# Optimization experiments

Hardware: AMD Instinct MI355X
Metric: run time of the kernel (lower is better)

## Reference

```python
import jax, jax.numpy as jnp
import numpy as np

N_HEAD = 16
EPS = 1e-06


def setup_inputs() -> dict:
    key = jax.random.key(0)
    ks = jax.random.split(key, 9)
    B, S, Q, D, Dp = 16, 4096, 49, 1024, 1024
    INIT = 0.02  # GPT-2 style init scale keeps exp(scores) finite
    x = jax.random.normal(ks[0], (B, S, D), dtype=jnp.float32)
    y = jax.random.normal(ks[1], (B, Q, Dp), dtype=jnp.float32)
    # multiplicative binary mask applied to exp(scores), shaped [1,1,49,S//64,64]
    attention_mask = (jax.random.uniform(ks[2], (1, 1, Q, S // 64, 64)) > 0.5).astype(jnp.float32)
    W_attn = jax.random.normal(ks[3], (D, 2 * D), dtype=jnp.float32) * INIT
    b_attn = jnp.zeros((2 * D,), dtype=jnp.float32)
    W_mlp = jax.random.normal(ks[4], (Dp, D), dtype=jnp.float32) * INIT
    b_mlp = jnp.zeros((D,), dtype=jnp.float32)
    W_proj = jax.random.normal(ks[5], (D, Dp), dtype=jnp.float32) * INIT
    b_proj = jnp.zeros((Dp,), dtype=jnp.float32)
    return {"x": x, "y": y, "attention_mask": attention_mask,
            "W_attn": W_attn, "b_attn": b_attn, "W_mlp": W_mlp, "b_mlp": b_mlp,
            "W_proj": W_proj, "b_proj": b_proj}


def reference(x, y, attention_mask, W_attn, b_attn, W_mlp, b_mlp, W_proj, b_proj):
    B, S, D = x.shape
    Q = y.shape[1]
    H = N_HEAD
    hd = D // H
    # c_attn (Conv1D): x @ W + b -> split into key, value
    kv = x @ W_attn + b_attn                       # [B,S,2D]
    key, value = kv[..., :D], kv[..., D:]
    k = key.reshape(B, S, H, hd).transpose(0, 2, 3, 1)    # [B,H,hd,S] (k=True perm)
    v = value.reshape(B, S, H, hd).transpose(0, 2, 1, 3)  # [B,H,S,hd]
    q = (y @ W_mlp + b_mlp).reshape(B, Q, H, hd).transpose(0, 2, 1, 3)  # [B,H,Q,hd]
    # fp32 scores, scaled by sqrt(head_dim)
    w = jnp.einsum('bhqd,bhds->bhqs', q.astype(jnp.float32), k.astype(jnp.float32))
    w = w / jnp.sqrt(jnp.float32(hd))
    # custom exp + multiplicative blocked mask + epsilon-stabilized normalize
    e = (jnp.exp(w).reshape(B, H, 49, -1, 64) * attention_mask).reshape(B, H, Q, S)
    w = e / (e.sum(-1, keepdims=True) + EPS)
    # PV matmul, cast to bf16 as in the original, then merge heads
    a = jnp.einsum('bhqs,bhsd->bhqd', w, v.astype(jnp.float32)).astype(jnp.bfloat16)
    a = a.transpose(0, 2, 1, 3).reshape(B, Q, D).astype(jnp.float32)
    out = a @ W_proj + b_proj                      # c_proj
    return out
```

## Files before the change

kernel.cpp:

```cpp
#include <hip/hip_runtime.h>
#include <cstdint>

typedef __bf16 bf16x8 __attribute__((ext_vector_type(8)));
typedef float f32x4 __attribute__((ext_vector_type(4)));
typedef unsigned short u16;

#define GBAR() asm volatile("s_barrier" ::: "memory")
#define SBAR0() __builtin_amdgcn_sched_barrier(0)
#define LGKM0() do { asm volatile("s_waitcnt lgkmcnt(0)" ::: "memory"); SBAR0(); } while (0)
#define VM6()  asm volatile("s_waitcnt vmcnt(6)" ::: "memory")
#define VM8()  asm volatile("s_waitcnt vmcnt(8)" ::: "memory")
#define MFMA16(a, b, c) __builtin_amdgcn_mfma_f32_16x16x32_bf16((a), (b), (c), 0, 0, 0)

__device__ __forceinline__ u16 f2bf(float f) {
  unsigned u = __builtin_bit_cast(unsigned, f);
  u += 0x7fffu + ((u >> 16) & 1u);
  return (u16)(u >> 16);
}
__device__ __forceinline__ float bfu(ushort4 v, int r) {
  unsigned short s = (r == 0) ? v.x : (r == 1) ? v.y : (r == 2) ? v.z : v.w;
  return __builtin_bit_cast(float, (unsigned)s << 16);
}

__global__ void cast_f32_bf16(const float* __restrict__ in, u16* __restrict__ out,
                              int n4) {
  int i = blockIdx.x * blockDim.x + threadIdx.x;
  int stride = gridDim.x * blockDim.x;
  for (; i < n4; i += stride) {
    float4 v = ((const float4*)in)[i];
    ushort4 o;
    o.x = f2bf(v.x); o.y = f2bf(v.y); o.z = f2bf(v.z); o.w = f2bf(v.w);
    ((ushort4*)out)[i] = o;
  }
}

__global__ void transpose_all(const float* __restrict__ Wa, const float* __restrict__ Wm,
                              const float* __restrict__ Wp,
                              u16* __restrict__ oa, u16* __restrict__ om,
                              u16* __restrict__ op) {
  __shared__ float t[64][65];
  int z = blockIdx.z;
  const float* in = (z == 0) ? Wa : (z == 1) ? Wm : Wp;
  u16* out = (z == 0) ? oa : (z == 1) ? om : op;
  int C = (z == 0) ? 2048 : 1024;
  const int R = 1024;
  if (blockIdx.x * 64 >= C) return;
  int tc = blockIdx.x * 64, tr = blockIdx.y * 64;
  int c = threadIdx.x & 63, r0 = threadIdx.x >> 6;
  #pragma unroll
  for (int p = 0; p < 16; ++p) {
    int r = p * 4 + r0;
    t[r][c] = in[(long)(tr + r) * C + (tc + c)];
  }
  __syncthreads();
  #pragma unroll
  for (int p = 0; p < 16; ++p) {
    int r = p * 4 + r0;
    out[(long)(tc + r) * R + (tr + c)] = f2bf(t[c][r]);
  }
}

__global__ void mask_prep(const float* __restrict__ in, u16* __restrict__ out) {
  __shared__ float t[64][65];
  int s0 = blockIdx.x * 64;
  int c = threadIdx.x & 63, r0 = threadIdx.x >> 6;
  #pragma unroll
  for (int p = 0; p < 16; ++p) {
    int q = p * 4 + r0;
    t[q][c] = (q < 49) ? in[(long)q * 4096 + s0 + c] : 0.f;
  }
  __syncthreads();
  #pragma unroll
  for (int p = 0; p < 16; ++p) {
    int r = p * 4 + r0;
    out[(long)(s0 + r) * 64 + c] = f2bf(t[c][r]);
  }
}

template<int MODE>
__global__ __launch_bounds__(512, 2) void gemm256(
    const u16* __restrict__ A, const u16* __restrict__ BT,
    const float* __restrict__ bias, void* __restrict__ outp)
{
  __shared__ __align__(16) char lds[131072];

  int tid = threadIdx.x;
  int l = tid & 63, w = tid >> 6;
  int wr = w >> 2, wc = w & 3;
  int lr = l & 15, lh = l >> 4;

  int bid = blockIdx.x;
  int mt, nt;
  long out_off = 0;
  const u16* Ap = A;
  const u16* BTp = BT;
  if constexpr (MODE == 0) {
    int wg = (bid & 7) * 128 + (bid >> 3);
    mt = wg >> 2; nt = wg & 3;
  } else {
    int wg = (bid & 7) * 8 + (bid >> 3);
    mt = wg & 3; nt = wg >> 2;
    int b = blockIdx.y;
    BTp = BT + (long)b * 4194304;
    out_off = (long)b * 4194304;
  }
  long Arow0 = (long)mt * 256;
  long Brow0 = (long)nt * 256;

  int rho = (w << 3) + (l >> 3);
  int csw = ((l & 7) ^ (l >> 3)) << 3;
  const u16* agA = Ap + (Arow0 + rho) * 1024 + csw;
  int browoff = (w >> 2) * 64 + (w & 3) * 8 + (l >> 3);
  const u16* agB = BTp + (Brow0 + browoff) * 1024 + csw;
  char* ldsAthr = lds + rho * 128 + (l & 7) * 16;
  char* ldsBthr = lds + 32768 + browoff * 128 + (l & 7) * 16;

  auto SA = [&](int dt, int st, int mh) {
    char* d = ldsAthr + (dt & 1) * 65536 + mh * 8192;
    const u16* s = agA + (long)st * 64 + mh * 65536;
    __builtin_amdgcn_global_load_lds(
        (const __attribute__((address_space(1))) void*)s,
        (__attribute__((address_space(3))) void*)d, 16, 0, 0);
    __builtin_amdgcn_global_load_lds(
        (const __attribute__((address_space(1))) void*)(s + 131072),
        (__attribute__((address_space(3))) void*)(d + 16384), 16, 0, 0);
  };
  auto SB = [&](int dt, int st, int h) {
    char* d = ldsBthr + (dt & 1) * 65536 + h * 4096;
    const u16* s = agB + (long)st * 64 + h * 32768;
    __builtin_amdgcn_global_load_lds(
        (const __attribute__((address_space(1))) void*)s,
        (__attribute__((address_space(3))) void*)d, 16, 0, 0);
    __builtin_amdgcn_global_load_lds(
        (const __attribute__((address_space(1))) void*)(s + 131072),
        (__attribute__((address_space(3))) void*)(d + 16384), 16, 0, 0);
  };

  int arow_b = (wr * 128 + lr) * 128;
  int brow_b = (wc * 64 + lr) * 128 + 32768;
  int xr0 = (lh ^ (lr & 7)) << 4;
  int xr1 = ((4 + lh) ^ (lr & 7)) << 4;

  f32x4 acc[8][4];
  #pragma unroll
  for (int m = 0; m < 8; ++m)
    #pragma unroll
    for (int n = 0; n < 4; ++n) acc[m][n] = f32x4{0.f, 0.f, 0.f, 0.f};

  bf16x8 af[4][2], bn0[2][2], bn1[2][2];

  auto RD_AF0 = [&](int buf) {
    #pragma unroll
    for (int m = 0; m < 4; ++m) {
      af[m][0] = *(const bf16x8*)(lds + buf + arow_b + m * 2048 + xr0);
      af[m][1] = *(const bf16x8*)(lds + buf + arow_b + m * 2048 + xr1);
    }
  };
  auto RD_AF1 = [&](int buf) {
    #pragma unroll
    for (int m = 0; m < 4; ++m) {
      af[m][0] = *(const bf16x8*)(lds + buf + arow_b + 8192 + m * 2048 + xr0);
      af[m][1] = *(const bf16x8*)(lds + buf + arow_b + 8192 + m * 2048 + xr1);
    }
  };
  auto RD_BN0 = [&](int buf) {
    #pragma unroll
    for (int n = 0; n < 2; ++n) {
      bn0[n][0] = *(const bf16x8*)(lds + buf + brow_b + n * 2048 + xr0);
      bn0[n][1] = *(const bf16x8*)(lds + buf + brow_b + n * 2048 + xr1);
    }
  };
  auto RD_BN1 = [&](int buf) {
    #pragma unroll
    for (int n = 0; n < 2; ++n) {
      bn1[n][0] = *(const bf16x8*)(lds + buf + brow_b + 4096 + n * 2048 + xr0);
      bn1[n][1] = *(const bf16x8*)(lds + buf + brow_b + 4096 + n * 2048 + xr1);
    }
  };
  auto Q = [&](int mo, int no, bf16x8 (&bn)[2][2]) {
    __builtin_amdgcn_s_setprio(1);
    #pragma unroll
    for (int m = 0; m < 4; ++m)
      #pragma unroll
      for (int n = 0; n < 2; ++n) {
        acc[mo + m][no + n] = MFMA16(af[m][0], bn[n][0], acc[mo + m][no + n]);
        acc[mo + m][no + n] = MFMA16(af[m][1], bn[n][1], acc[mo + m][no + n]);
      }
    __builtin_amdgcn_s_setprio(0);
  };

  SA(0, 0, 0); SA(0, 0, 1); SB(0, 0, 0); SB(0, 0, 1);
  SA(1, 1, 0); SA(1, 1, 1); SB(1, 1, 0);
  VM6(); GBAR();

  for (int i = 0; i < 8; ++i) {
    int t = 2 * i;
    RD_AF0(0); RD_BN0(0); SBAR0();
    SB(t + 1, t + 1, 1);
    GBAR(); LGKM0();
    Q(0, 0, bn0);
    GBAR();
    RD_BN1(0); SBAR0();
    { int tt = t + 2; SA(tt, tt < 16 ? tt : 15, 0); }
    GBAR(); LGKM0();
    Q(0, 2, bn1);
    GBAR();
    RD_AF1(0); SBAR0();
    { int tt = t + 2; SB(tt, tt < 16 ? tt : 15, 0); }
    GBAR(); LGKM0();
    Q(4, 0, bn0);
    GBAR();
    { int tt = t + 2; SA(tt, tt < 16 ? tt : 15, 1); }
    GBAR(); VM6();
    Q(4, 2, bn1);
    GBAR();
    RD_AF0(65536); RD_BN0(65536); SBAR0();
    { int tt = t + 2; SB(tt, tt < 16 ? tt : 15, 1); }
    GBAR(); LGKM0();
    Q(0, 0, bn0);
    GBAR();
    RD_BN1(65536); SBAR0();
    { int tt = t + 3; SA(tt, tt < 16 ? tt : 15, 0); }
    GBAR(); LGKM0();
    Q(0, 2, bn1);
    GBAR();
    RD_AF1(65536); SBAR0();
    { int tt = t + 3; SB(tt, tt < 16 ? tt : 15, 0); }
    GBAR(); LGKM0();
    Q(4, 0, bn0);
    GBAR();
    { int tt = t + 3; SA(tt, tt < 16 ? tt : 15, 1); }
    GBAR(); VM6();
    Q(4, 2, bn1);
    GBAR();
  }

  asm volatile("s_waitcnt vmcnt(0)" ::: "memory");

  #pragma unroll
  for (int m = 0; m < 8; ++m) {
    #pragma unroll
    for (int n = 0; n < 4; ++n) {
      #pragma unroll
      for (int r = 0; r < 4; ++r) {
        long row = Arow0 + wr * 128 + m * 16 + lh * 4 + r;
        long col = Brow0 + wc * 64 + n * 16 + lr;
        float v = acc[m][n][r];
        if constexpr (MODE == 0) {
          v += bias[col];
          long addr = (row >> 12) * 4194304 + (col >> 6) * 262144
                    + (row & 4095) * 64 + (col & 63);
          ((u16*)outp)[addr] = f2bf(v);
        } else {
          v += bias[1024 + row];
          ((u16*)outp)[out_off + row * 4096 + col] = f2bf(v);
        }
      }
    }
  }
}

template<int MODE>
__global__ __launch_bounds__(256, 4) void gemm64(
    const void* __restrict__ Ap, const u16* __restrict__ BT,
    const float* __restrict__ bias, void* __restrict__ outp)
{
  __shared__ u16 As[64][64];
  __shared__ u16 Bs[64][64];

  int bid = blockIdx.x;
  int mt = bid >> 4, nt = bid & 15;
  int tid = threadIdx.x;
  int l = tid & 63, w = tid >> 6;
  int wr = w >> 1, wc = w & 1;
  int lr = l & 15, lh = l >> 4;

  f32x4 acc[2][2];
  #pragma unroll
  for (int m = 0; m < 2; ++m)
    #pragma unroll
    for (int n = 0; n < 2; ++n) acc[m][n] = f32x4{0.f, 0.f, 0.f, 0.f};

  long arow0 = (long)mt * 64;
  long brow0 = (long)nt * 64;
  int srow = tid >> 3, sc = tid & 7;

  for (int kt = 0; kt < 16; ++kt) {
    int ko = kt * 64;
    #pragma unroll
    for (int p = 0; p < 2; ++p) {
      int row = srow + p * 32;
      int cs = (sc ^ (row & 7)) << 3;
      __builtin_amdgcn_global_load_lds(
          (const __attribute__((address_space(1))) void*)(BT + (brow0 + row) * 1024 + ko + cs),
          (__attribute__((address_space(3))) void*)(&Bs[row][sc * 8]), 16, 0, 0);
      if constexpr (MODE == 3)
        __builtin_amdgcn_global_load_lds(
            (const __attribute__((address_space(1))) void*)((const u16*)Ap + (arow0 + row) * 1024 + ko + cs),
            (__attribute__((address_space(3))) void*)(&As[row][sc * 8]), 16, 0, 0);
    }
    if constexpr (MODE == 2) {
      #pragma unroll
      for (int p = 0; p < 2; ++p) {
        int row = srow + p * 32;
        int cs = (sc ^ (row & 7)) << 3;
        ushort4 o0 = {0, 0, 0, 0}, o1 = {0, 0, 0, 0};
        if (arow0 + row < 784) {
          const float* src = (const float*)Ap + (arow0 + row) * 1024 + ko + cs;
          float4 f0 = *(const float4*)src;
          float4 f1 = *(const float4*)(src + 4);
          o0.x = f2bf(f0.x); o0.y = f2bf(f0.y); o0.z = f2bf(f0.z); o0.w = f2bf(f0.w);
          o1.x = f2bf(f1.x); o1.y = f2bf(f1.y); o1.z = f2bf(f1.z); o1.w = f2bf(f1.w);
        }
        *(ushort4*)(&As[row][sc * 8]) = o0;
        *(ushort4*)(&As[row][sc * 8 + 4]) = o1;
      }
    }
    __syncthreads();
    #pragma unroll
    for (int kk = 0; kk < 2; ++kk) {
      bf16x8 afr[2], bfr[2];
      #pragma unroll
      for (int m = 0; m < 2; ++m) {
        int row = wr * 32 + m * 16 + lr;
        afr[m] = *(const bf16x8*)((const char*)&As[row][0] + (((kk * 4 + lh) ^ (row & 7)) << 4));
      }
      #pragma unroll
      for (int n = 0; n < 2; ++n) {
        int row = wc * 32 + n * 16 + lr;
        bfr[n] = *(const bf16x8*)((const char*)&Bs[row][0] + (((kk * 4 + lh) ^ (row & 7)) << 4));
      }
      #pragma unroll
      for (int m = 0; m < 2; ++m)
        #pragma unroll
        for (int n = 0; n < 2; ++n)
          acc[m][n] = MFMA16(afr[m], bfr[n], acc[m][n]);
    }
    __syncthreads();
  }

  #pragma unroll
  for (int m = 0; m < 2; ++m) {
    #pragma unroll
    for (int n = 0; n < 2; ++n) {
      #pragma unroll
      for (int r = 0; r < 4; ++r) {
        int row = (int)arow0 + wr * 32 + m * 16 + lh * 4 + r;
        int col = (int)brow0 + wc * 32 + n * 16 + lr;
        if (row < 784) {
          float v = acc[m][n][r] + bias[col];
          if constexpr (MODE == 2) {
            int b = row / 49, qi = row - b * 49;
            long addr = ((long)(b * 16 + (col >> 6)) * 64 + qi) * 64 + (col & 63);
            ((u16*)outp)[addr] = f2bf(v);
          } else {
            ((float*)outp)[(long)row * 1024 + col] = v;
          }
        }
      }
    }
  }
}

__global__ __launch_bounds__(256, 4) void attn_part(
    const u16* __restrict__ Kt, const u16* __restrict__ Vt, const u16* __restrict__ Q,
    const u16* __restrict__ maskT,
    float* __restrict__ partA, float* __restrict__ prs)
{
  __shared__ __align__(16) char lds[40960];

  int bh = blockIdx.x, chunk = blockIdx.y;
  int tid = threadIdx.x;
  int l = tid & 63, w = tid >> 6;
  int lr = l & 15, lh = l >> 4;

  const u16* Kb = Kt + (long)bh * 262144;
  const u16* Vb = Vt + (long)bh * 262144;
  const u16* Qb = Q + (long)bh * 4096;

  int t0 = chunk * 16;
  const int nt = 16;
  int tmax = t0 + nt - 1;

  int strow = tid >> 3;
  int sc = tid & 7;

  auto STAGE = [&](int buf, int tt) {
    long s0 = (long)tt * 64;
    #pragma unroll
    for (int h = 0; h < 2; ++h) {
      int row = h * 32 + strow;
      int cs = (sc ^ (row & 7)) << 3;
      const u16* ksrc = Kb + (s0 + row) * 64 + cs;
      char* kdst = lds + buf * 8192 + row * 128 + sc * 16;
      __builtin_amdgcn_global_load_lds(
          (const __attribute__((address_space(1))) void*)ksrc,
          (__attribute__((address_space(3))) void*)kdst, 16, 0, 0);
      const u16* vsrc = Vb + (long)row * 4096 + s0 + cs;
      char* vdst = lds + 16384 + buf * 8192 + row * 128 + sc * 16;
      __builtin_amdgcn_global_load_lds(
          (const __attribute__((address_space(1))) void*)vsrc,
          (__attribute__((address_space(3))) void*)vdst, 16, 0, 0);
    }
  };

  bf16x8 qf[2];
  #pragma unroll
  for (int kf2 = 0; kf2 < 2; ++kf2)
    qf[kf2] = *(const bf16x8*)(Qb + (w * 16 + lr) * 64 + kf2 * 32 + lh * 8);

  bf16x8 ones;
  #pragma unroll
  for (int j = 0; j < 8; ++j) ones[j] = (__bf16)1.0f;

  f32x4 acc_a[4];
  #pragma unroll
  for (int n = 0; n < 4; ++n) acc_a[n] = f32x4{0.f, 0.f, 0.f, 0.f};
  f32x4 acc_rs = f32x4{0.f, 0.f, 0.f, 0.f};

  char* Pw = lds + 32768 + w * 2048;
  const u16* mbase = maskT + w * 16 + lh * 4;

  STAGE(0, t0);
  STAGE(1, t0 + 1);
  ushort4 mvu[4];
  #pragma unroll
  for (int sf = 0; sf < 4; ++sf)
    mvu[sf] = *(const ushort4*)(mbase + ((long)t0 * 64 + sf * 16 + lr) * 64);
  VM8();
  GBAR();

  for (int it = 0; it < nt; ++it) {
    int buf = it & 1;
    const char* Kl = lds + buf * 8192;
    const char* Vl = lds + 16384 + buf * 8192;

    int tn = it + 1 < nt ? t0 + it + 1 : tmax;
    ushort4 mvn[4];
    #pragma unroll
    for (int sf = 0; sf < 4; ++sf)
      mvn[sf] = *(const ushort4*)(mbase + ((long)tn * 64 + sf * 16 + lr) * 64);

    bf16x8 kf[4][2];
    #pragma unroll
    for (int sf = 0; sf < 4; ++sf) {
      int srw = sf * 16 + lr;
      int xb = srw & 7;
      kf[sf][0] = *(const bf16x8*)(Kl + srw * 128 + ((lh ^ xb) << 4));
      kf[sf][1] = *(const bf16x8*)(Kl + srw * 128 + (((4 + lh) ^ xb) << 4));
    }
    f32x4 lg[4];
    #pragma unroll
    for (int sf = 0; sf < 4; ++sf) {
      f32x4 t = f32x4{0.f, 0.f, 0.f, 0.f};
      t = MFMA16(qf[0], kf[sf][0], t);
      t = MFMA16(qf[1], kf[sf][1], t);
      lg[sf] = t;
    }

    bf16x8 vf[2][4];
    #pragma unroll
    for (int k2 = 0; k2 < 2; ++k2)
      #pragma unroll
      for (int n = 0; n < 4; ++n) {
        int vrow = n * 16 + lr;
        vf[k2][n] = *(const bf16x8*)(Vl + vrow * 128 + (((k2 * 4 + lh) ^ (lr & 7)) << 4));
      }

    #pragma unroll
    for (int sf = 0; sf < 4; ++sf) {
      #pragma unroll
      for (int r = 0; r < 4; ++r) {
        int qq = lh * 4 + r;
        float e = __expf(lg[sf][r] * 0.125f) * bfu(mvu[sf], r);
        int byte = (qq * 128 + (sf * 16 + lr) * 2) ^ ((qq & 7) << 4);
        *(u16*)(Pw + byte) = f2bf(e);
      }
    }

    #pragma unroll
    for (int k2 = 0; k2 < 2; ++k2) {
      int byte = (lr * 128 + k2 * 64 + lh * 16) ^ ((lr & 7) << 4);
      bf16x8 pf;
      __builtin_memcpy(&pf, Pw + byte, 16);
      #pragma unroll
      for (int n = 0; n < 4; ++n)
        acc_a[n] = MFMA16(pf, vf[k2][n], acc_a[n]);
      acc_rs = MFMA16(pf, ones, acc_rs);
    }

    LGKM0();
    GBAR();
    { int tt = it + 2 < nt ? t0 + it + 2 : tmax; STAGE(buf, tt); }
    VM8();
    GBAR();

    #pragma unroll
    for (int sf = 0; sf < 4; ++sf) mvu[sf] = mvn[sf];
  }

  long base = ((long)bh * 4 + chunk) * 64;
  #pragma unroll
  for (int r = 0; r < 4; ++r) {
    int q = w * 16 + lh * 4 + r;
    if (lr == 0) prs[base + q] = acc_rs[r];
    #pragma unroll
    for (int n = 0; n < 4; ++n)
      partA[(base + q) * 64 + n * 16 + lr] = acc_a[n][r];
  }
}

__global__ __launch_bounds__(256) void attn_reduce(
    const float* __restrict__ partA, const float* __restrict__ prs,
    u16* __restrict__ Abf)
{
  int bh = blockIdx.x;
  int t = threadIdx.x;
  int q = t >> 2, d0 = (t & 3) * 16;
  if (q >= 49) return;
  int b = bh >> 4, h = bh & 15;

  float rs = 1e-6f;
  #pragma unroll
  for (int c = 0; c < 4; ++c) rs += prs[((long)bh * 4 + c) * 64 + q];

  #pragma unroll
  for (int j = 0; j < 4; ++j) {
    float4 s = float4{0.f, 0.f, 0.f, 0.f};
    #pragma unroll
    for (int c = 0; c < 4; ++c) {
      float4 v = *(const float4*)(partA + (((long)bh * 4 + c) * 64 + q) * 64 + d0 + j * 4);
      s.x += v.x; s.y += v.y; s.z += v.z; s.w += v.w;
    }
    ushort4 o;
    o.x = f2bf(s.x / rs); o.y = f2bf(s.y / rs);
    o.z = f2bf(s.z / rs); o.w = f2bf(s.w / rs);
    *(ushort4*)(Abf + ((long)(b * 49 + q) * 1024 + h * 64 + d0 + j * 4)) = o;
  }
}

extern "C" void kernel_launch(void* const* d_in, const int* in_sizes, int n_in,
                              void* d_out, int out_size, void* d_ws, size_t ws_size,
                              hipStream_t stream) {
  const float* x      = (const float*)d_in[0];
  const float* y      = (const float*)d_in[1];
  const float* mask   = (const float*)d_in[2];
  const float* W_attn = (const float*)d_in[3];
  const float* b_attn = (const float*)d_in[4];
  const float* W_mlp  = (const float*)d_in[5];
  const float* b_mlp  = (const float*)d_in[6];
  const float* W_proj = (const float*)d_in[7];
  const float* b_proj = (const float*)d_in[8];

  if (ws_size < 417333248ULL) return;

  char* ws = (char*)d_ws;
  u16* x_bf    = (u16*)(ws);
  u16* Kt      = (u16*)(ws + 134217728L);
  u16* Vt      = (u16*)(ws + 268435456L);
  u16* WT_attn = (u16*)(ws + 402653184L);
  u16* WT_mlp  = (u16*)(ws + 406847488L);
  u16* WT_proj = (u16*)(ws + 408944640L);
  u16* q_ws    = (u16*)(ws + 412876800L);
  u16* a_bf    = (u16*)(ws + 414973952L);
  u16* maskT   = (u16*)(ws + 416808960L);
  float* partA = (float*)(ws);
  float* prs   = (float*)(ws + 16777216L);

  cast_f32_bf16<<<2048, 256, 0, stream>>>(x, x_bf, 16777216);
  transpose_all<<<dim3(32, 16, 3), 256, 0, stream>>>(W_attn, W_mlp, W_proj,
                                                     WT_attn, WT_mlp, WT_proj);
  mask_prep<<<64, 256, 0, stream>>>(mask, maskT);

  gemm256<0><<<1024, 512, 0, stream>>>(x_bf, WT_attn, b_attn, Kt);
  gemm256<1><<<dim3(64, 16), 512, 0, stream>>>(WT_attn + 1048576, x_bf, b_attn, Vt);
  gemm64<2><<<224, 256, 0, stream>>>(y, WT_mlp, b_mlp, q_ws);

  attn_part<<<dim3(256, 4), 256, 0, stream>>>(Kt, Vt, q_ws, maskT, partA, prs);
  attn_reduce<<<256, 256, 0, stream>>>(partA, prs, a_bf);

  gemm64<3><<<224, 256, 0, stream>>>(a_bf, WT_proj, b_proj, d_out);
}
```

Baseline: 465.4 us.

## Stage only activation tile in LDS with triple buffering, read weights from global

The 256x256 bf16 GEMM now copies only the activation operand into LDS, using three 32KB buffers filled with global_load_lds two k-steps ahead. The weight operand fragments are loaded straight from global memory into registers each k-step. The fine-grained half-tile schedule with many barriers becomes one loop step per 64-wide k-slice with a single barrier. This cuts LDS footprint, LDS traffic and barrier count, but exposes global-load latency on the weight fragments. It also relies on implicit vmcnt waits to make sure the staged LDS buffers have landed before they are read.

```diff
diff --git a/kernel.cpp b/kernel.cpp
--- a/kernel.cpp
+++ b/kernel.cpp
@@ -8,7 +8,6 @@
 #define GBAR() asm volatile("s_barrier" ::: "memory")
 #define SBAR0() __builtin_amdgcn_sched_barrier(0)
 #define LGKM0() do { asm volatile("s_waitcnt lgkmcnt(0)" ::: "memory"); SBAR0(); } while (0)
-#define VM6()  asm volatile("s_waitcnt vmcnt(6)" ::: "memory")
 #define VM8()  asm volatile("s_waitcnt vmcnt(8)" ::: "memory")
 #define MFMA16(a, b, c) __builtin_amdgcn_mfma_f32_16x16x32_bf16((a), (b), (c), 0, 0, 0)
 
@@ -82,7 +81,7 @@
     const u16* __restrict__ A, const u16* __restrict__ BT,
     const float* __restrict__ bias, void* __restrict__ outp)
 {
-  __shared__ __align__(16) char lds[131072];
+  __shared__ __align__(16) char lds[98304];
 
   int tid = threadIdx.x;
   int l = tid & 63, w = tid >> 6;
@@ -107,37 +106,29 @@
   long Arow0 = (long)mt * 256;
   long Brow0 = (long)nt * 256;
 
+  const u16* xbase = (MODE == 0) ? Ap : BTp;
+  long xrow0 = (MODE == 0) ? Arow0 : Brow0;
   int rho = (w << 3) + (l >> 3);
   int csw = ((l & 7) ^ (l >> 3)) << 3;
-  const u16* agA = Ap + (Arow0 + rho) * 1024 + csw;
-  int browoff = (w >> 2) * 64 + (w & 3) * 8 + (l >> 3);
-  const u16* agB = BTp + (Brow0 + browoff) * 1024 + csw;
-  char* ldsAthr = lds + rho * 128 + (l & 7) * 16;
-  char* ldsBthr = lds + 32768 + browoff * 128 + (l & 7) * 16;
-
-  auto SA = [&](int dt, int st, int mh) {
-    char* d = ldsAthr + (dt & 1) * 65536 + mh * 8192;
-    const u16* s = agA + (long)st * 64 + mh * 65536;
-    __builtin_amdgcn_global_load_lds(
-        (const __attribute__((address_space(1))) void*)s,
-        (__attribute__((address_space(3))) void*)d, 16, 0, 0);
-    __builtin_amdgcn_global_load_lds(
-        (const __attribute__((address_space(1))) void*)(s + 131072),
-        (__attribute__((address_space(3))) void*)(d + 16384), 16, 0, 0);
+  const u16* xg = xbase + (xrow0 + rho) * 1024 + csw;
+  char* ldsthr = lds + rho * 128 + (l & 7) * 16;
+
+  auto STAGE_X = [&](int bi, int st) {
+    char* d = ldsthr + bi * 32768;
+    const u16* s = xg + (long)st * 64;
+    #pragma unroll
+    for (int q = 0; q < 4; ++q)
+      __builtin_amdgcn_global_load_lds(
+          (const __attribute__((address_space(1))) void*)(s + (long)q * 65536),
+          (__attribute__((address_space(3))) void*)(d + q * 8192), 16, 0, 0);
   };
-  auto SB = [&](int dt, int st, int h) {
-    char* d = ldsBthr + (dt & 1) * 65536 + h * 4096;
-    const u16* s = agB + (long)st * 64 + h * 32768;
-    __builtin_amdgcn_global_load_lds(
-        (const __attribute__((address_space(1))) void*)s,
-        (__attribute__((address_space(3))) void*)d, 16, 0, 0);
-    __builtin_amdgcn_global_load_lds(
-        (const __attribute__((address_space(1))) void*)(s + 131072),
-        (__attribute__((address_space(3))) void*)(d + 16384), 16, 0, 0);
-  };
+
+  const u16* wgp = (MODE == 0)
+      ? BTp + (Brow0 + wc * 64 + lr) * 1024 + lh * 8
+      : Ap  + (Arow0 + wr * 128 + lr) * 1024 + lh * 8;
 
   int arow_b = (wr * 128 + lr) * 128;
-  int brow_b = (wc * 64 + lr) * 128 + 32768;
+  int brow_b = (wc * 64 + lr) * 128;
   int xr0 = (lh ^ (lr & 7)) << 4;
   int xr1 = ((4 + lh) ^ (lr & 7)) << 4;
 
@@ -149,34 +140,6 @@
 
   bf16x8 af[4][2], bn0[2][2], bn1[2][2];
 
-  auto RD_AF0 = [&](int buf) {
-    #pragma unroll
-    for (int m = 0; m < 4; ++m) {
-      af[m][0] = *(const bf16x8*)(lds + buf + arow_b + m * 2048 + xr0);
-      af[m][1] = *(const bf16x8*)(lds + buf + arow_b + m * 2048 + xr1);
-    }
-  };
-  auto RD_AF1 = [&](int buf) {
-    #pragma unroll
-    for (int m = 0; m < 4; ++m) {
-      af[m][0] = *(const bf16x8*)(lds + buf + arow_b + 8192 + m * 2048 + xr0);
-      af[m][1] = *(const bf16x8*)(lds + buf + arow_b + 8192 + m * 2048 + xr1);
-    }
-  };
-  auto RD_BN0 = [&](int buf) {
-    #pragma unroll
-    for (int n = 0; n < 2; ++n) {
-      bn0[n][0] = *(const bf16x8*)(lds + buf + brow_b + n * 2048 + xr0);
-      bn0[n][1] = *(const bf16x8*)(lds + buf + brow_b + n * 2048 + xr1);
-    }
-  };
-  auto RD_BN1 = [&](int buf) {
-    #pragma unroll
-    for (int n = 0; n < 2; ++n) {
-      bn1[n][0] = *(const bf16x8*)(lds + buf + brow_b + 4096 + n * 2048 + xr0);
-      bn1[n][1] = *(const bf16x8*)(lds + buf + brow_b + 4096 + n * 2048 + xr1);
-    }
-  };
   auto Q = [&](int mo, int no, bf16x8 (&bn)[2][2]) {
     __builtin_amdgcn_s_setprio(1);
     #pragma unroll
@@ -189,53 +152,70 @@
     __builtin_amdgcn_s_setprio(0);
   };
 
-  SA(0, 0, 0); SA(0, 0, 1); SB(0, 0, 0); SB(0, 0, 1);
-  SA(1, 1, 0); SA(1, 1, 1); SB(1, 1, 0);
-  VM6(); GBAR();
-
-  for (int i = 0; i < 8; ++i) {
-    int t = 2 * i;
-    RD_AF0(0); RD_BN0(0); SBAR0();
-    SB(t + 1, t + 1, 1);
-    GBAR(); LGKM0();
-    Q(0, 0, bn0);
+  STAGE_X(0, 0);
+  STAGE_X(1, 1);
+  asm volatile("s_waitcnt vmcnt(4)" ::: "memory");
+  GBAR();
+
+  int cur = 0;
+  for (int t = 0; t < 16; ++t) {
+    int buf = cur * 32768;
+    if constexpr (MODE == 0) {
+      #pragma unroll
+      for (int n = 0; n < 2; ++n)
+        #pragma unroll
+        for (int h = 0; h < 2; ++h) {
+          bn0[n][h] = *(const bf16x8*)(wgp + n * 16384 + t * 64 + h * 32);
+          bn1[n][h] = *(const bf16x8*)(wgp + (n + 2) * 16384 + t * 64 + h * 32);
+        }
+      SBAR0();
+      #pragma unroll
+      for (int m = 0; m < 4; ++m) {
+        af[m][0] = *(const bf16x8*)(lds + buf + arow_b + m * 2048 + xr0);
+        af[m][1] = *(const bf16x8*)(lds + buf + arow_b + m * 2048 + xr1);
+      }
+      LGKM0();
+      Q(0, 0, bn0); Q(0, 2, bn1);
+      #pragma unroll
+      for (int m = 0; m < 4; ++m) {
+        af[m][0] = *(const bf16x8*)(lds + buf + arow_b + 8192 + m * 2048 + xr0);
+        af[m][1] = *(const bf16x8*)(lds + buf + arow_b + 8192 + m * 2048 + xr1);
+      }
+      LGKM0();
+      Q(4, 0, bn0); Q(4, 2, bn1);
+    } else {
+      #pragma unroll
+      for (int m = 0; m < 4; ++m)
+        #pragma unroll
+        for (int h = 0; h < 2; ++h)
+          af[m][h] = *(const bf16x8*)(wgp + m * 16384 + t * 64 + h * 32);
+      SBAR0();
+      #pragma unroll
+      for (int n = 0; n < 2; ++n) {
+        bn0[n][0] = *(const bf16x8*)(lds + buf + brow_b + n * 2048 + xr0);
+        bn0[n][1] = *(const bf16x8*)(lds + buf + brow_b + n * 2048 + xr1);
+        bn1[n][0] = *(const bf16x8*)(lds + buf + brow_b + 4096 + n * 2048 + xr0);
+        bn1[n][1] = *(const bf16x8*)(lds + buf + brow_b + 4096 + n * 2048 + xr1);
+      }
+      LGKM0();
+      Q(0, 0, bn0); Q(0, 2, bn1);
+      #pragma unroll
+      for (int m = 0; m < 4; ++m)
+        #pragma unroll
+        for (int h = 0; h < 2; ++h)
+          af[m][h] = *(const bf16x8*)(wgp + 65536 + m * 16384 + t * 64 + h * 32);
+      Q(4, 0, bn0); Q(4, 2, bn1);
+    }
     GBAR();
-    RD_BN1(0); SBAR0();
-    { int tt = t + 2; SA(tt, tt < 16 ? tt : 15, 0); }
-    GBAR(); LGKM0();
-    Q(0, 2, bn1);
-    GBAR();
-    RD_AF1(0); SBAR0();
-    { int tt = t + 2; SB(tt, tt < 16 ? tt : 15, 0); }
-    GBAR(); LGKM0();
-    Q(4, 0, bn0);
-    GBAR();
-    { int tt = t + 2; SA(tt, tt < 16 ? tt : 15, 1); }
-    GBAR(); VM6();
-    Q(4, 2, bn1);
-    GBAR();
-    RD_AF0(65536); RD_BN0(65536); SBAR0();
-    { int tt = t + 2; SB(tt, tt < 16 ? tt : 15, 1); }
-    GBAR(); LGKM0();
-    Q(0, 0, bn0);
-    GBAR();
-    RD_BN1(65536); SBAR0();
-    { int tt = t + 3; SA(tt, tt < 16 ? tt : 15, 0); }
-    GBAR(); LGKM0();
-    Q(0, 2, bn1);
-    GBAR();
-    RD_AF1(65536); SBAR0();
-    { int tt = t + 3; SB(tt, tt < 16 ? tt : 15, 0); }
-    GBAR(); LGKM0();
-    Q(4, 0, bn0);
-    GBAR();
-    { int tt = t + 3; SA(tt, tt < 16 ? tt : 15, 1); }
-    GBAR(); VM6();
-    Q(4, 2, bn1);
-    GBAR();
-  }
-
-  asm volatile("s_waitcnt vmcnt(0)" ::: "memory");
+    {
+      int st = t + 2;
+      int bs = cur + 2; if (bs >= 3) bs -= 3;
+      STAGE_X(bs, st < 16 ? st : 15);
+    }
+    ++cur; if (cur == 3) cur = 0;
+  }
+
+  asm volatile("s_waitcnt vmcnt(0) lgkmcnt(0)" ::: "memory");
 
   #pragma unroll
   for (int m = 0; m < 8; ++m) {
```

New measurement: 743.4 us. 1.6x slower.
